# Performance work log

Hardware: AMD Instinct MI355X
Metric: run time of the kernel (lower is better)

## Reference

```python
import jax, jax.numpy as jnp
import numpy as np

N, E, NC = 50000, 800000, 5
H, C = 4, 16      # branch GATConvs: heads=4, out=16 -> 64
H2, C2 = 4, 32    # conv2/conv3: heads=4, out=32 -> 128
HID = 128


def _gat(x, src, dst, W, a_s, a_d, b, mask=None, edge_attr=None, We=None, a_e=None):
    """PyG-style GATConv with add_self_loops=True (fill_value='mean' for edge_attr)."""
    n = x.shape[0]
    h, c = a_s.shape
    hx = (x @ W).reshape(n, h, c)                      # [N,H,C]
    as_n = (hx * a_s).sum(-1)                          # [N,H]
    ad_n = (hx * a_d).sum(-1)                          # [N,H]
    alpha = as_n[src] + ad_n[dst]                      # [E,H]
    loop = as_n + ad_n                                 # self-loop scores [N,H]
    if edge_attr is not None:
        ee = (edge_attr @ We).reshape(-1, h, c)        # [E,H,C]
        alpha = alpha + (ee * a_e).sum(-1)
        w = mask.astype(x.dtype) if mask is not None else jnp.ones((edge_attr.shape[0],), x.dtype)
        # fill_value='mean': self-loop attr = mean of (masked) incoming edge_attr
        loop_attr = jax.ops.segment_sum(edge_attr * w[:, None], dst, n) / \
                    jnp.maximum(jax.ops.segment_sum(w, dst, n), 1.0)[:, None]
        loop = loop + ((loop_attr @ We).reshape(n, h, c) * a_e).sum(-1)
    alpha = jax.nn.leaky_relu(alpha, 0.2)
    loop = jax.nn.leaky_relu(loop, 0.2)
    if mask is not None:
        alpha = jnp.where(mask[:, None], alpha, -jnp.inf)
    # segment softmax over destination neighborhoods (self-loop always present)
    m = jnp.maximum(jax.ops.segment_max(alpha, dst, n), loop)      # [N,H], finite
    ex = jnp.exp(alpha - m[dst])                                   # [E,H]
    if mask is not None:
        ex = jnp.where(mask[:, None], ex, 0.0)
    exl = jnp.exp(loop - m)                                        # [N,H]
    denom = jax.ops.segment_sum(ex, dst, n) + exl
    out = jax.ops.segment_sum(ex[:, :, None] * hx[src], dst, n) + exl[:, :, None] * hx
    return (out / denom[:, :, None]).reshape(n, h * c) + b


def setup_inputs() -> dict:
    key = jax.random.key(0)
    ks = iter(jax.random.split(key, 64))
    def nrm(shape, s=0.1):
        return jax.random.normal(next(ks), shape, jnp.float32) * s
    d = {}
    d["x"] = nrm((N, 1), 1.0)
    d["edge_index"] = jax.random.randint(next(ks), (2, E), 0, N, jnp.int32)
    d["edge_attr"] = nrm((E, 3), 1.0)
    d["mask_t"] = jax.random.randint(next(ks), (E,), 0, 2, jnp.int32).astype(bool)
    d["mask_g"] = jax.random.randint(next(ks), (E,), 0, 2, jnp.int32).astype(bool)
    d["mask_p"] = jax.random.randint(next(ks), (E,), 0, 2, jnp.int32).astype(bool)
    for p in ("t", "g", "p"):
        d[f"W{p}"] = nrm((1, H * C))
        d[f"a{p}s"] = nrm((H, C)); d[f"a{p}d"] = nrm((H, C)); d[f"a{p}e"] = nrm((H, C))
        d[f"W{p}e"] = nrm((3, H * C))
        d[f"b{p}"] = jnp.zeros((H * C,), jnp.float32)
    d["Wf"] = nrm((3 * H * C, HID)); d["bf"] = jnp.zeros((HID,), jnp.float32)
    d["W2"] = nrm((HID, H2 * C2)); d["a2s"] = nrm((H2, C2)); d["a2d"] = nrm((H2, C2)); d["b2"] = jnp.zeros((H2 * C2,), jnp.float32)
    d["W3"] = nrm((HID, H2 * C2)); d["a3s"] = nrm((H2, C2)); d["a3d"] = nrm((H2, C2)); d["b3"] = jnp.zeros((H2 * C2,), jnp.float32)
    d["Wc1"] = nrm((HID, HID // 2)); d["bc1"] = jnp.zeros((HID // 2,), jnp.float32)
    d["Wc2"] = nrm((HID // 2, NC)); d["bc2"] = jnp.zeros((NC,), jnp.float32)
    return d


def reference(x, edge_index, edge_attr, mask_t, mask_g, mask_p,
              Wt, ats, atd, ate, Wte, bt,
              Wg, ags, agd, age, Wge, bg,
              Wp, aps, apd, ape, Wpe, bp,
              Wf, bf, W2, a2s, a2d, b2, W3, a3s, a3d, b3,
              Wc1, bc1, Wc2, bc2):
    src, dst = edge_index[0], edge_index[1]
    ht = _gat(x, src, dst, Wt, ats, atd, bt, mask_t, edge_attr, Wte, ate)
    hg = _gat(x, src, dst, Wg, ags, agd, bg, mask_g, edge_attr, Wge, age)
    hp = _gat(x, src, dst, Wp, aps, apd, bp, mask_p, edge_attr, Wpe, ape)
    h = jax.nn.relu(jnp.concatenate([ht, hg, hp], -1) @ Wf + bf)
    h = jax.nn.relu(_gat(h, src, dst, W2, a2s, a2d, b2))
    h = jax.nn.relu(_gat(h, src, dst, W3, a3s, a3d, b3))
    logits = jax.nn.relu(h @ Wc1 + bc1) @ Wc2 + bc2
    return jax.nn.log_softmax(logits, -1)
```

## Files before the change

kernel.cpp:

```cpp
#include <hip/hip_runtime.h>
#include <hip/hip_bf16.h>

#define LEAKY(v) ((v) > 0.f ? (v) : 0.2f * (v))

__device__ __forceinline__ unsigned short f_to_bf16(float f) {
    union { float f; unsigned int i; } v; v.f = f;
    unsigned int x = v.i;
    return (unsigned short)((x + 0x7fffu + ((x >> 16) & 1u)) >> 16);
}

__device__ __forceinline__ float2 bf2_to_f2(unsigned int u) {
    union { unsigned int i; float f; } a, b;
    a.i = (u & 0xffffu) << 16;
    b.i = u & 0xffff0000u;
    float2 r; r.x = a.f; r.y = b.f;
    return r;
}

struct ConstBuf {
    float ws[3][4];
    float wd[3][4];
    float M[3][3][4];
    float G[12][128];
    float bias2[128];
};
#define CB_FLOATS 1724

struct BranchW { const float *W, *as_, *ad_, *ae, *We, *b; };
struct PreArgs { BranchW br[3]; const float *Wf, *bf; ConstBuf* cb; };

__global__ void k_precompute(PreArgs A) {
    int t = threadIdx.x;
    if (t < 24) {
        int b = t / 8, r = t % 8, h = r & 3; bool isd = r >= 4;
        const float* a = isd ? A.br[b].ad_ : A.br[b].as_;
        float s = 0.f;
        for (int c = 0; c < 16; ++c) s += A.br[b].W[h * 16 + c] * a[h * 16 + c];
        if (isd) A.cb->wd[b][h] = s; else A.cb->ws[b][h] = s;
    }
    if (t >= 32 && t < 68) {
        int id = t - 32, b = id / 12, k = (id % 12) / 4, h = id & 3;
        float s = 0.f;
        for (int c = 0; c < 16; ++c) s += A.br[b].We[k * 64 + h * 16 + c] * A.br[b].ae[h * 16 + c];
        A.cb->M[b][k][h] = s;
    }
    if (t >= 128) {
        int j = t - 128;
        float s = A.bf[j];
        for (int b = 0; b < 3; ++b)
            for (int i = 0; i < 64; ++i)
                s += A.br[b].b[i] * A.Wf[(b * 64 + i) * 128 + j];
        A.cb->bias2[j] = s;
    }
    for (int id = t; id < 1536; id += 256) {
        int r = id >> 7, j = id & 127, b = r >> 2, h = r & 3;
        float s = 0.f;
        for (int c = 0; c < 16; ++c)
            s += A.br[b].W[h * 16 + c] * A.Wf[(b * 64 + h * 16 + c) * 128 + j];
        A.cb->G[r][j] = s;
    }
}

__global__ void k_count(const int* __restrict__ ei, int E, int* __restrict__ deg) {
    int e = blockIdx.x * blockDim.x + threadIdx.x;
    if (e < E) atomicAdd(&deg[ei[E + e]], 1);
}

#define SCAN_EPB 2048

__global__ void k_scan1(const int* __restrict__ deg, int* __restrict__ off,
                        int* __restrict__ partials, int total) {
    __shared__ int sd[256];
    int t = threadIdx.x;
    int base = blockIdx.x * SCAN_EPB + t * 8;
    int v[8];
    int s = 0;
    #pragma unroll
    for (int i = 0; i < 8; ++i) {
        int idx = base + i;
        v[i] = (idx < total - 1) ? deg[idx] : 0;
        s += v[i];
    }
    sd[t] = s;
    __syncthreads();
    #pragma unroll
    for (int ofs = 1; ofs < 256; ofs <<= 1) {
        int u = (t >= ofs) ? sd[t - ofs] : 0;
        __syncthreads();
        sd[t] += u;
        __syncthreads();
    }
    if (t == 255) partials[blockIdx.x] = sd[255];
    int run = sd[t] - s;
    #pragma unroll
    for (int i = 0; i < 8; ++i) {
        int idx = base + i;
        if (idx < total) off[idx] = run;
        run += v[i];
    }
}

__global__ void k_scan2(int* __restrict__ partials, int nb) {
    __shared__ int sd[256];
    int t = threadIdx.x;
    int v = (t < nb) ? partials[t] : 0;
    sd[t] = v;
    __syncthreads();
    #pragma unroll
    for (int ofs = 1; ofs < 256; ofs <<= 1) {
        int u = (t >= ofs) ? sd[t - ofs] : 0;
        __syncthreads();
        sd[t] += u;
        __syncthreads();
    }
    if (t < nb) partials[t] = sd[t] - v;
}

__global__ void k_scan3(int* __restrict__ off, const int* __restrict__ partials,
                        int* __restrict__ cursor, int total) {
    int idx = blockIdx.x * blockDim.x + threadIdx.x;
    if (idx < total) {
        int v = off[idx] + partials[idx / SCAN_EPB];
        off[idx] = v;
        if (idx < total - 1) cursor[idx] = v;
    }
}

__global__ void k_scatter(const int* __restrict__ ei, const float* __restrict__ attr,
                          const int* __restrict__ mt, const int* __restrict__ mg,
                          const int* __restrict__ mp, int E, int* __restrict__ cursor,
                          float4* __restrict__ rec) {
    int e = blockIdx.x * blockDim.x + threadIdx.x;
    if (e < E) {
        int d = ei[E + e];
        int p = atomicAdd(&cursor[d], 1);
        float4 r;
        r.x = attr[e * 3 + 0];
        r.y = attr[e * 3 + 1];
        r.z = attr[e * 3 + 2];
        unsigned int bits = (mt[e] != 0 ? 1u : 0u) | (mg[e] != 0 ? 2u : 0u) | (mp[e] != 0 ? 4u : 0u);
        unsigned int packed = (unsigned int)ei[e] | (bits << 16);
        r.w = __int_as_float((int)packed);
        rec[p] = r;
    }
}

__global__ void k_branch(const float* __restrict__ x, const int* __restrict__ off,
                         const float4* __restrict__ rec, int* __restrict__ csr_src,
                         const ConstBuf* __restrict__ cb, float* __restrict__ h1, int N) {
    __shared__ float sc[CB_FLOATS];
    for (int i = threadIdx.x; i < CB_FLOATS; i += 256) sc[i] = ((const float*)cb)[i];
    __syncthreads();
    int g = threadIdx.x >> 4, l = threadIdx.x & 15;
    int n = blockIdx.x * 16 + g;
    if (n >= N) return;

    float num[12], den[12], asum[9], cnt[3];
    #pragma unroll
    for (int i = 0; i < 12; ++i) { num[i] = 0.f; den[i] = 0.f; }
    #pragma unroll
    for (int i = 0; i < 9; ++i) asum[i] = 0.f;
    cnt[0] = cnt[1] = cnt[2] = 0.f;

    float xn = x[n];
    int beg = off[n], end = off[n + 1];
    for (int p = beg + l; p < end; p += 16) {
        float4 r = rec[p];
        unsigned int packed = (unsigned int)__float_as_int(r.w);
        int src = (int)(packed & 0xffffu);
        unsigned int bits = packed >> 16;
        csr_src[p] = src;
        float xs = x[src];
        float a0 = r.x, a1 = r.y, a2 = r.z;
        #pragma unroll
        for (int b = 0; b < 3; ++b) {
            if ((bits >> b) & 1u) {
                cnt[b] += 1.f;
                asum[b * 3 + 0] += a0; asum[b * 3 + 1] += a1; asum[b * 3 + 2] += a2;
                #pragma unroll
                for (int h = 0; h < 4; ++h) {
                    float al = xs * sc[b * 4 + h] + xn * sc[12 + b * 4 + h]
                             + a0 * sc[24 + b * 12 + 0 + h]
                             + a1 * sc[24 + b * 12 + 4 + h]
                             + a2 * sc[24 + b * 12 + 8 + h];
                    al = LEAKY(al);
                    float ex = __expf(al);
                    den[b * 4 + h] += ex;
                    num[b * 4 + h] += ex * xs;
                }
            }
        }
    }
    #pragma unroll
    for (int m = 1; m < 16; m <<= 1) {
        #pragma unroll
        for (int i = 0; i < 12; ++i) {
            num[i] += __shfl_xor(num[i], m, 64);
            den[i] += __shfl_xor(den[i], m, 64);
        }
        #pragma unroll
        for (int i = 0; i < 9; ++i) asum[i] += __shfl_xor(asum[i], m, 64);
        #pragma unroll
        for (int i = 0; i < 3; ++i) cnt[i] += __shfl_xor(cnt[i], m, 64);
    }
    float S[12];
    #pragma unroll
    for (int b = 0; b < 3; ++b) {
        float inv = 1.f / fmaxf(cnt[b], 1.f);
        float l0 = asum[b * 3 + 0] * inv, l1 = asum[b * 3 + 1] * inv, l2 = asum[b * 3 + 2] * inv;
        #pragma unroll
        for (int h = 0; h < 4; ++h) {
            float lp = xn * (sc[b * 4 + h] + sc[12 + b * 4 + h])
                     + l0 * sc[24 + b * 12 + 0 + h]
                     + l1 * sc[24 + b * 12 + 4 + h]
                     + l2 * sc[24 + b * 12 + 8 + h];
            lp = LEAKY(lp);
            float exl = __expf(lp);
            float sden = den[b * 4 + h] + exl;
            S[b * 4 + h] = (num[b * 4 + h] + exl * xn) / sden;
        }
    }
    int jb = l * 8;
    float o[8];
    #pragma unroll
    for (int q = 0; q < 8; ++q) {
        int j = jb + q;
        float a = sc[60 + 1536 + j];
        #pragma unroll
        for (int k = 0; k < 12; ++k) a += S[k] * sc[60 + k * 128 + j];
        o[q] = fmaxf(a, 0.f);
    }
    float4* dst = (float4*)(h1 + (size_t)n * 128 + jb);
    dst[0] = make_float4(o[0], o[1], o[2], o[3]);
    dst[1] = make_float4(o[4], o[5], o[6], o[7]);
}

__global__ void k_mm128s(const float* __restrict__ A, const float* __restrict__ W,
                         const float* __restrict__ a_s, const float* __restrict__ a_d,
                         unsigned short* __restrict__ hxb, float* __restrict__ as_,
                         float* __restrict__ ad_, int N) {
    __shared__ float As[8 * 128];
    int j = threadIdx.x;
    int n0 = blockIdx.x * 8;
    #pragma unroll
    for (int i = 0; i < 8; ++i) {
        int n = n0 + i;
        As[i * 128 + j] = (n < N) ? A[(size_t)n * 128 + j] : 0.f;
    }
    __syncthreads();
    float acc[8] = {0.f, 0.f, 0.f, 0.f, 0.f, 0.f, 0.f, 0.f};
    const float4* As4 = (const float4*)As;
    for (int k = 0; k < 128; k += 4) {
        float w0 = W[(k + 0) * 128 + j];
        float w1 = W[(k + 1) * 128 + j];
        float w2 = W[(k + 2) * 128 + j];
        float w3 = W[(k + 3) * 128 + j];
        #pragma unroll
        for (int i = 0; i < 8; ++i) {
            float4 h4 = As4[(i * 128 + k) >> 2];
            acc[i] += h4.x * w0 + h4.y * w1 + h4.z * w2 + h4.w * w3;
        }
    }
    float asj = a_s[j], adj = a_d[j];
    int h = j >> 5;
    #pragma unroll
    for (int i = 0; i < 8; ++i) {
        int n = n0 + i;
        if (n < N) hxb[(size_t)n * 128 + j] = f_to_bf16(acc[i]);
        float vs = acc[i] * asj, vd = acc[i] * adj;
        #pragma unroll
        for (int m = 1; m < 32; m <<= 1) {
            vs += __shfl_xor(vs, m, 64);
            vd += __shfl_xor(vd, m, 64);
        }
        if ((j & 31) == 0 && n < N) {
            as_[(size_t)n * 4 + h] = vs;
            ad_[(size_t)n * 4 + h] = vd;
        }
    }
}

__global__ void k_gatagg(const unsigned short* __restrict__ hxb, const float* __restrict__ as_,
                         const float* __restrict__ ad_, const float* __restrict__ b,
                         const int* __restrict__ off, const int* __restrict__ csr_src,
                         float* __restrict__ out, int N) {
    int wave = threadIdx.x >> 6, lane = threadIdx.x & 63;
    int n = blockIdx.x * 4 + wave;
    if (n >= N) return;
    int h = lane >> 4;
    int lofs = lane * 2;
    float adn = ad_[(size_t)n * 4 + h];
    int beg = off[n], end = off[n + 1];
    float acc0 = 0.f, acc1 = 0.f, accd = 0.f;
    for (int p = beg; p < end; p += 8) {
        int s[8]; float e[8]; unsigned int u[8]; bool valid[8];
        #pragma unroll
        for (int i = 0; i < 8; ++i) {
            valid[i] = (p + i < end);
            int q = valid[i] ? (p + i) : beg;
            s[i] = csr_src[q];
        }
        #pragma unroll
        for (int i = 0; i < 8; ++i) e[i] = as_[(size_t)s[i] * 4 + h];
        #pragma unroll
        for (int i = 0; i < 8; ++i) u[i] = *(const unsigned int*)(hxb + (size_t)s[i] * 128 + lofs);
        #pragma unroll
        for (int i = 0; i < 8; ++i) {
            float ex = valid[i] ? __expf(LEAKY(e[i] + adn)) : 0.f;
            float2 v = bf2_to_f2(u[i]);
            acc0 += ex * v.x; acc1 += ex * v.y; accd += ex;
        }
    }
    float aln = LEAKY(as_[(size_t)n * 4 + h] + adn);
    float exl = __expf(aln);
    unsigned int un = *(const unsigned int*)(hxb + (size_t)n * 128 + lofs);
    float2 vn = bf2_to_f2(un);
    float inv = 1.f / (accd + exl);
    float o0 = (acc0 + exl * vn.x) * inv + b[lofs + 0];
    float o1 = (acc1 + exl * vn.y) * inv + b[lofs + 1];
    float2 r; r.x = fmaxf(o0, 0.f); r.y = fmaxf(o1, 0.f);
    *(float2*)(out + (size_t)n * 128 + lofs) = r;
}

#define CLS_NPB 32
__global__ void k_cls(const float* __restrict__ h3, const float* __restrict__ Wc1,
                      const float* __restrict__ bc1, const float* __restrict__ Wc2,
                      const float* __restrict__ bc2, float* __restrict__ out, int N) {
    __shared__ float hs[CLS_NPB * 128];
    int tid = threadIdx.x;
    int nb = blockIdx.x * CLS_NPB;
    for (int i = tid; i < CLS_NPB * 128; i += 256) {
        int n = nb + (i >> 7);
        hs[i] = (n < N) ? h3[(size_t)n * 128 + (i & 127)] : 0.f;
    }
    __syncthreads();
    int g = tid >> 6, j = tid & 63;
    const float4* hb4 = (const float4*)(hs + g * 8 * 128);
    float bj = bc1[j];
    float acc[8];
    #pragma unroll
    for (int i = 0; i < 8; ++i) acc[i] = bj;
    for (int k = 0; k < 128; k += 4) {
        float w0 = Wc1[(k + 0) * 64 + j];
        float w1 = Wc1[(k + 1) * 64 + j];
        float w2 = Wc1[(k + 2) * 64 + j];
        float w3 = Wc1[(k + 3) * 64 + j];
        #pragma unroll
        for (int i = 0; i < 8; ++i) {
            float4 h4 = hb4[(i * 128 + k) >> 2];
            acc[i] += h4.x * w0 + h4.y * w1 + h4.z * w2 + h4.w * w3;
        }
    }
    float w2v[5];
    #pragma unroll
    for (int c = 0; c < 5; ++c) w2v[c] = Wc2[j * 5 + c];
    #pragma unroll
    for (int i = 0; i < 8; ++i) {
        float t = fmaxf(acc[i], 0.f);
        float p[5];
        #pragma unroll
        for (int c = 0; c < 5; ++c) p[c] = t * w2v[c];
        #pragma unroll
        for (int m = 1; m < 64; m <<= 1) {
            #pragma unroll
            for (int c = 0; c < 5; ++c) p[c] += __shfl_xor(p[c], m, 64);
        }
        if (j == 0) {
            int n = nb + g * 8 + i;
            if (n < N) {
                float l[5], mx = -1e30f;
                #pragma unroll
                for (int c = 0; c < 5; ++c) { l[c] = p[c] + bc2[c]; mx = fmaxf(mx, l[c]); }
                float s = 0.f;
                #pragma unroll
                for (int c = 0; c < 5; ++c) s += __expf(l[c] - mx);
                float lse = mx + __logf(s);
                #pragma unroll
                for (int c = 0; c < 5; ++c) out[(size_t)n * 5 + c] = l[c] - lse;
            }
        }
    }
}

extern "C" void kernel_launch(void* const* d_in, const int* in_sizes, int n_in,
                              void* d_out, int out_size, void* d_ws, size_t ws_size,
                              hipStream_t stream) {
    const float* x    = (const float*)d_in[0];
    const int*   ei   = (const int*)d_in[1];
    const float* attr = (const float*)d_in[2];
    const int*   mt   = (const int*)d_in[3];
    const int*   mg   = (const int*)d_in[4];
    const int*   mp   = (const int*)d_in[5];
    const float* Wf   = (const float*)d_in[24];
    const float* bf   = (const float*)d_in[25];
    const float* W2   = (const float*)d_in[26];
    const float* a2s  = (const float*)d_in[27];
    const float* a2d  = (const float*)d_in[28];
    const float* b2   = (const float*)d_in[29];
    const float* W3   = (const float*)d_in[30];
    const float* a3s  = (const float*)d_in[31];
    const float* a3d  = (const float*)d_in[32];
    const float* b3   = (const float*)d_in[33];
    const float* Wc1  = (const float*)d_in[34];
    const float* bc1  = (const float*)d_in[35];
    const float* Wc2  = (const float*)d_in[36];
    const float* bc2  = (const float*)d_in[37];

    int N = in_sizes[0];
    int E = in_sizes[1] / 2;

    char* w = (char*)d_ws;
    auto alloc = [&](size_t bytes) {
        char* p = w;
        w += (bytes + 255) & ~(size_t)255;
        return p;
    };
    int* off      = (int*)alloc((size_t)(N + 1) * 4);
    int* cursor   = (int*)alloc((size_t)N * 4);
    int* deg      = (int*)alloc((size_t)N * 4);
    int* partials = (int*)alloc(1024 * 4);
    int* csr_src  = (int*)alloc((size_t)E * 4);
    ConstBuf* cb  = (ConstBuf*)alloc(sizeof(ConstBuf));
    float* as_    = (float*)alloc((size_t)N * 4 * 4);
    float* ad_    = (float*)alloc((size_t)N * 4 * 4);
    float* bufA   = (float*)alloc((size_t)N * 128 * 4);
    float4* rec   = (float4*)alloc((size_t)E * 16);
    unsigned short* hxb = (unsigned short*)alloc((size_t)N * 256);

    PreArgs pa;
    for (int b = 0; b < 3; ++b) {
        pa.br[b].W   = (const float*)d_in[6 + b * 6 + 0];
        pa.br[b].as_ = (const float*)d_in[6 + b * 6 + 1];
        pa.br[b].ad_ = (const float*)d_in[6 + b * 6 + 2];
        pa.br[b].ae  = (const float*)d_in[6 + b * 6 + 3];
        pa.br[b].We  = (const float*)d_in[6 + b * 6 + 4];
        pa.br[b].b   = (const float*)d_in[6 + b * 6 + 5];
    }
    pa.Wf = Wf; pa.bf = bf; pa.cb = cb;

    int total = N + 1;
    int nScanBlocks = (total + SCAN_EPB - 1) / SCAN_EPB;

    hipMemsetAsync(deg, 0, (size_t)N * 4, stream);
    hipLaunchKernelGGL(k_precompute, dim3(1), dim3(256), 0, stream, pa);
    int gE = (E + 255) / 256;
    hipLaunchKernelGGL(k_count, dim3(gE), dim3(256), 0, stream, ei, E, deg);
    hipLaunchKernelGGL(k_scan1, dim3(nScanBlocks), dim3(256), 0, stream, deg, off, partials, total);
    hipLaunchKernelGGL(k_scan2, dim3(1), dim3(256), 0, stream, partials, nScanBlocks);
    hipLaunchKernelGGL(k_scan3, dim3((total + 255) / 256), dim3(256), 0, stream,
                       off, partials, cursor, total);
    hipLaunchKernelGGL(k_scatter, dim3(gE), dim3(256), 0, stream,
                       ei, attr, mt, mg, mp, E, cursor, rec);
    hipLaunchKernelGGL(k_branch, dim3((N + 15) / 16), dim3(256), 0, stream,
                       x, off, rec, csr_src, cb, bufA, N);
    hipLaunchKernelGGL(k_mm128s, dim3((N + 7) / 8), dim3(128), 0, stream,
                       bufA, W2, a2s, a2d, hxb, as_, ad_, N);
    hipLaunchKernelGGL(k_gatagg, dim3((N + 3) / 4), dim3(256), 0, stream,
                       hxb, as_, ad_, b2, off, csr_src, bufA, N);
    hipLaunchKernelGGL(k_mm128s, dim3((N + 7) / 8), dim3(128), 0, stream,
                       bufA, W3, a3s, a3d, hxb, as_, ad_, N);
    hipLaunchKernelGGL(k_gatagg, dim3((N + 3) / 4), dim3(256), 0, stream,
                       hxb, as_, ad_, b3, off, csr_src, bufA, N);
    hipLaunchKernelGGL(k_cls, dim3((N + CLS_NPB - 1) / CLS_NPB), dim3(256), 0, stream,
                       bufA, Wc1, bc1, Wc2, bc2, (float*)d_out, N);
}
```

Baseline: 497.3 us.

## Use bf16 MFMA for 128x128 GAT projections with a separate score kernel

The scalar FP32 matmul kernel for the conv2/conv3 projections is replaced by a bf16 MFMA kernel (16x16x32). Each block handles 64 rows, and the weights are pre-swizzled into MFMA fragment layout by a small prep kernel. Attention scores are now computed in a separate kernel from the bf16 hx output rather than fused into the matmul epilogue. This cuts ALU-bound FP32 work, at the cost of extra launches, an extra read of hx, and bf16 rounding of both inputs and scores.

```diff
diff --git a/kernel.cpp b/kernel.cpp
--- a/kernel.cpp
+++ b/kernel.cpp
@@ -2,6 +2,10 @@
 #include <hip/hip_bf16.h>
 
 #define LEAKY(v) ((v) > 0.f ? (v) : 0.2f * (v))
+
+typedef __attribute__((ext_vector_type(8))) short s8;
+typedef __attribute__((ext_vector_type(4))) float f4;
+typedef __attribute__((ext_vector_type(4))) unsigned short us4;
 
 __device__ __forceinline__ unsigned short f_to_bf16(float f) {
     union { float f; unsigned int i; } v; v.f = f;
@@ -58,6 +62,15 @@
         for (int c = 0; c < 16; ++c)
             s += A.br[b].W[h * 16 + c] * A.Wf[(b * 64 + h * 16 + c) * 128 + j];
         A.cb->G[r][j] = s;
+    }
+}
+
+__global__ void k_prepw(const float* __restrict__ W, unsigned short* __restrict__ out) {
+    for (int i = threadIdx.x; i < 16384; i += 256) {
+        int j = i & 7, lane = (i >> 3) & 63, kk = (i >> 9) & 3, ct = i >> 11;
+        int k = kk * 32 + (lane >> 4) * 8 + j;
+        int n = ct * 16 + (lane & 15);
+        out[i] = f_to_bf16(W[k * 128 + n]);
     }
 }
 
@@ -235,49 +248,77 @@
     dst[1] = make_float4(o[4], o[5], o[6], o[7]);
 }
 
-__global__ void k_mm128s(const float* __restrict__ A, const float* __restrict__ W,
-                         const float* __restrict__ a_s, const float* __restrict__ a_d,
-                         unsigned short* __restrict__ hxb, float* __restrict__ as_,
-                         float* __restrict__ ad_, int N) {
-    __shared__ float As[8 * 128];
-    int j = threadIdx.x;
-    int n0 = blockIdx.x * 8;
+__global__ void k_mm128b(const float* __restrict__ A, const unsigned short* __restrict__ wf,
+                         unsigned short* __restrict__ hxb, int N) {
+    __shared__ unsigned short sA[64 * 136];
+    __shared__ unsigned short sW[16384];
+    int tid = threadIdx.x;
+    int base = blockIdx.x * 64;
+    const float4* wf4 = (const float4*)wf;
+    float4* sW4 = (float4*)sW;
+    #pragma unroll
+    for (int i = 0; i < 8; ++i) sW4[tid + i * 256] = wf4[tid + i * 256];
     #pragma unroll
     for (int i = 0; i < 8; ++i) {
-        int n = n0 + i;
-        As[i * 128 + j] = (n < N) ? A[(size_t)n * 128 + j] : 0.f;
+        int f = tid + i * 256;
+        int row = f >> 5, c4 = f & 31;
+        int n = base + row;
+        float4 v = (n < N) ? ((const float4*)A)[(size_t)n * 32 + c4]
+                           : make_float4(0.f, 0.f, 0.f, 0.f);
+        us4 b;
+        b.x = f_to_bf16(v.x); b.y = f_to_bf16(v.y);
+        b.z = f_to_bf16(v.z); b.w = f_to_bf16(v.w);
+        *(us4*)(&sA[row * 136 + c4 * 4]) = b;
     }
     __syncthreads();
-    float acc[8] = {0.f, 0.f, 0.f, 0.f, 0.f, 0.f, 0.f, 0.f};
-    const float4* As4 = (const float4*)As;
-    for (int k = 0; k < 128; k += 4) {
-        float w0 = W[(k + 0) * 128 + j];
-        float w1 = W[(k + 1) * 128 + j];
-        float w2 = W[(k + 2) * 128 + j];
-        float w3 = W[(k + 3) * 128 + j];
-        #pragma unroll
-        for (int i = 0; i < 8; ++i) {
-            float4 h4 = As4[(i * 128 + k) >> 2];
-            acc[i] += h4.x * w0 + h4.y * w1 + h4.z * w2 + h4.w * w3;
-        }
-    }
-    float asj = a_s[j], adj = a_d[j];
-    int h = j >> 5;
-    #pragma unroll
-    for (int i = 0; i < 8; ++i) {
-        int n = n0 + i;
-        if (n < N) hxb[(size_t)n * 128 + j] = f_to_bf16(acc[i]);
-        float vs = acc[i] * asj, vd = acc[i] * adj;
-        #pragma unroll
-        for (int m = 1; m < 32; m <<= 1) {
-            vs += __shfl_xor(vs, m, 64);
-            vd += __shfl_xor(vd, m, 64);
-        }
-        if ((j & 31) == 0 && n < N) {
-            as_[(size_t)n * 4 + h] = vs;
-            ad_[(size_t)n * 4 + h] = vd;
-        }
-    }
+    int wv = tid >> 6, lane = tid & 63;
+    int q = lane >> 4, l15 = lane & 15;
+    int rowbase = wv * 16;
+    s8 af[4];
+    #pragma unroll
+    for (int kk = 0; kk < 4; ++kk)
+        af[kk] = *(const s8*)(&sA[(rowbase + l15) * 136 + kk * 32 + q * 8]);
+    #pragma unroll
+    for (int ct = 0; ct < 8; ++ct) {
+        f4 acc = {0.f, 0.f, 0.f, 0.f};
+        #pragma unroll
+        for (int kk = 0; kk < 4; ++kk) {
+            s8 bfr = *(const s8*)(&sW[((ct * 4 + kk) * 64 + lane) * 8]);
+            acc = __builtin_amdgcn_mfma_f32_16x16x32_bf16(af[kk], bfr, acc, 0, 0, 0);
+        }
+        #pragma unroll
+        for (int r = 0; r < 4; ++r) {
+            int n = base + rowbase + q * 4 + r;
+            if (n < N) hxb[(size_t)n * 128 + ct * 16 + l15] = f_to_bf16(acc[r]);
+        }
+    }
+}
+
+__global__ void k_scoresb(const unsigned short* __restrict__ hxb, const float* __restrict__ a_s,
+                          const float* __restrict__ a_d, float* __restrict__ as_,
+                          float* __restrict__ ad_, int N) {
+    __shared__ float sas[128], sad[128];
+    if (threadIdx.x < 128) { sas[threadIdx.x] = a_s[threadIdx.x]; sad[threadIdx.x] = a_d[threadIdx.x]; }
+    __syncthreads();
+    int tid = blockIdx.x * blockDim.x + threadIdx.x;
+    int n = tid >> 2, h = tid & 3;
+    if (n >= N) return;
+    const uint4* r4 = (const uint4*)(hxb + (size_t)n * 128 + h * 32);
+    float ss = 0.f, sd2 = 0.f;
+    #pragma unroll
+    for (int c = 0; c < 4; ++c) {
+        uint4 blob = r4[c];
+        unsigned int us[4] = { blob.x, blob.y, blob.z, blob.w };
+        #pragma unroll
+        for (int q = 0; q < 4; ++q) {
+            float2 v = bf2_to_f2(us[q]);
+            int col = h * 32 + c * 8 + q * 2;
+            ss  += v.x * sas[col] + v.y * sas[col + 1];
+            sd2 += v.x * sad[col] + v.y * sad[col + 1];
+        }
+    }
+    as_[(size_t)n * 4 + h] = ss;
+    ad_[(size_t)n * 4 + h] = sd2;
 }
 
 __global__ void k_gatagg(const unsigned short* __restrict__ hxb, const float* __restrict__ as_,
@@ -426,6 +467,8 @@
     float* bufA   = (float*)alloc((size_t)N * 128 * 4);
     float4* rec   = (float4*)alloc((size_t)E * 16);
     unsigned short* hxb = (unsigned short*)alloc((size_t)N * 256);
+    unsigned short* wf2 = (unsigned short*)alloc(16384 * 2);
+    unsigned short* wf3 = (unsigned short*)alloc(16384 * 2);
 
     PreArgs pa;
     for (int b = 0; b < 3; ++b) {
@@ -443,6 +486,8 @@
 
     hipMemsetAsync(deg, 0, (size_t)N * 4, stream);
     hipLaunchKernelGGL(k_precompute, dim3(1), dim3(256), 0, stream, pa);
+    hipLaunchKernelGGL(k_prepw, dim3(1), dim3(256), 0, stream, W2, wf2);
+    hipLaunchKernelGGL(k_prepw, dim3(1), dim3(256), 0, stream, W3, wf3);
     int gE = (E + 255) / 256;
     hipLaunchKernelGGL(k_count, dim3(gE), dim3(256), 0, stream, ei, E, deg);
     hipLaunchKernelGGL(k_scan1, dim3(nScanBlocks), dim3(256), 0, stream, deg, off, partials, total);
@@ -453,12 +498,16 @@
                        ei, attr, mt, mg, mp, E, cursor, rec);
     hipLaunchKernelGGL(k_branch, dim3((N + 15) / 16), dim3(256), 0, stream,
                        x, off, rec, csr_src, cb, bufA, N);
-    hipLaunchKernelGGL(k_mm128s, dim3((N + 7) / 8), dim3(128), 0, stream,
-                       bufA, W2, a2s, a2d, hxb, as_, ad_, N);
+    hipLaunchKernelGGL(k_mm128b, dim3((N + 63) / 64), dim3(256), 0, stream,
+                       bufA, wf2, hxb, N);
+    hipLaunchKernelGGL(k_scoresb, dim3(((size_t)N * 4 + 255) / 256), dim3(256), 0, stream,
+                       hxb, a2s, a2d, as_, ad_, N);
     hipLaunchKernelGGL(k_gatagg, dim3((N + 3) / 4), dim3(256), 0, stream,
                        hxb, as_, ad_, b2, off, csr_src, bufA, N);
-    hipLaunchKernelGGL(k_mm128s, dim3((N + 7) / 8), dim3(128), 0, stream,
-                       bufA, W3, a3s, a3d, hxb, as_, ad_, N);
+    hipLaunchKernelGGL(k_mm128b, dim3((N + 63) / 64), dim3(256), 0, stream,
+                       bufA, wf3, hxb, N);
+    hipLaunchKernelGGL(k_scoresb, dim3(((size_t)N * 4 + 255) / 256), dim3(256), 0, stream,
+                       hxb, a3s, a3d, as_, ad_, N);
     hipLaunchKernelGGL(k_gatagg, dim3((N + 3) / 4), dim3(256), 0, stream,
                        hxb, as_, ad_, b3, off, csr_src, bufA, N);
     hipLaunchKernelGGL(k_cls, dim3((N + CLS_NPB - 1) / CLS_NPB), dim3(256), 0, stream,
```

New measurement: 461.1 us. 7.3% less time.
